# Kernel tuning notes

Hardware: AMD Instinct MI355X
Metric: run time of the kernel (lower is better)

The kernel has to match this reference:

```python
import jax, jax.numpy as jnp
import numpy as np

NUM_HEADS = 8


def setup_inputs() -> dict:
    key = jax.random.key(0)
    N, D = 131072, 512
    ks = jax.random.split(key, 10)
    inv = 1.0 / np.sqrt(D)
    return {
        "unit_embeddings": jax.random.normal(ks[0], (N, D), dtype=jnp.float32),
        "mask": jnp.ones((N,), dtype=bool),
        "mil_query": jax.random.normal(ks[1], (D,), dtype=jnp.float32),
        "Wq": jax.random.uniform(ks[2], (D, D), jnp.float32, -inv, inv),
        "bq": jax.random.uniform(ks[3], (D,), jnp.float32, -inv, inv),
        "Wk": jax.random.uniform(ks[4], (D, D), jnp.float32, -inv, inv),
        "bk": jax.random.uniform(ks[5], (D,), jnp.float32, -inv, inv),
        "Wv": jax.random.uniform(ks[6], (D, D), jnp.float32, -inv, inv),
        "bv": jax.random.uniform(ks[7], (D,), jnp.float32, -inv, inv),
        "Wo": jax.random.uniform(ks[8], (D, D), jnp.float32, -inv, inv),
        "bo": jax.random.uniform(ks[9], (D,), jnp.float32, -inv, inv),
    }


def reference(unit_embeddings, mask, mil_query, Wq, bq, Wk, bk, Wv, bv, Wo, bo):
    N, D = unit_embeddings.shape
    H = NUM_HEADS
    hd = D // H
    scale = np.float32(np.sqrt(hd))
    # The torch module expands a single learned query to N copies and takes the
    # diagonal of the NxN per-head score matrix; mathematically scores[h,n] = q_h . k_h[n] / scale.
    q = mil_query @ Wq.T + bq                       # (D,)
    K = unit_embeddings @ Wk.T + bk                 # (N, D)
    V = unit_embeddings @ Wv.T + bv                 # (N, D)
    qh = q.reshape(H, hd)                           # (H, hd)
    Kh = K.reshape(N, H, hd)
    Vh = V.reshape(N, H, hd)
    scores = jnp.einsum('hd,nhd->hn', qh, Kh) / scale   # (H, N)
    scores = jnp.where(mask[None, :], scores, -jnp.inf)
    w = jax.nn.softmax(scores, axis=-1)             # (H, N); dropout is identity at eval
    weighted = jnp.einsum('hn,nhd->hd', w, Vh)      # (H, hd)
    # torch does .transpose(0,1).contiguous().view(D): flatten in (hd, H) order
    flat = weighted.T.reshape(D)
    package_embedding = flat @ Wo.T + bo            # (D,)
    final_attention_weights = w.mean(axis=0)        # (N,)
    return package_embedding, final_attention_weights
```

## Files before the change

### kernel.cpp

```cpp
#include <hip/hip_runtime.h>

#define NN 131072
#define DD 512
#define HH 8
#define NUNIT 2048

__device__ __forceinline__ float wave_sum64(float x) {
  float t;
#define DPPADD(ctrl)                                                                     \
  t = __int_as_float(__builtin_amdgcn_update_dpp(0, __float_as_int(x), ctrl, 0xf, 0xf, true)); \
  x += t;
  DPPADD(0x111)
  DPPADD(0x112)
  DPPADD(0x114)
  DPPADD(0x118)
  DPPADD(0x142)
  DPPADD(0x143)
#undef DPPADD
  return x;
}

__device__ __forceinline__ float rdlane(float v, int l) {
  return __int_as_float(__builtin_amdgcn_readlane(__float_as_int(v), l));
}

__device__ __forceinline__ float dpp_xor1(float x) {
  return __int_as_float(__builtin_amdgcn_update_dpp(0, __float_as_int(x), 0xB1, 0xf, 0xf, true));
}
__device__ __forceinline__ float dpp_xor2(float x) {
  return __int_as_float(__builtin_amdgcn_update_dpp(0, __float_as_int(x), 0x4E, 0xf, 0xf, true));
}

__global__ __launch_bounds__(256) void kA_q(const float* __restrict__ Wq,
                                            const float* __restrict__ bq,
                                            const float* __restrict__ mq,
                                            float* __restrict__ q) {
  int lane = threadIdx.x & 63;
  int gw = blockIdx.x * 4 + (threadIdx.x >> 6);
  const float4* wr = (const float4*)(Wq + (size_t)gw * DD);
  const float4* m4 = (const float4*)mq;
  float4 w0 = wr[lane], w1 = wr[64 + lane];
  float4 m0 = m4[lane], m1 = m4[64 + lane];
  float p = w0.x * m0.x + w0.y * m0.y + w0.z * m0.z + w0.w * m0.w +
            w1.x * m1.x + w1.y * m1.y + w1.z * m1.z + w1.w * m1.w;
  p = wave_sum64(p);
  if (lane == 63) q[gw] = p + bq[gw];
}

__global__ __launch_bounds__(256) void kB_kq(const float* __restrict__ Wk,
                                             const float* __restrict__ bk,
                                             const float* __restrict__ q,
                                             float* __restrict__ kq,
                                             float* __restrict__ cq) {
  int T = blockIdx.x * 256 + threadIdx.x;
  int h = T >> 9, j = T & 511;
  float acc = 0.f;
#pragma unroll 8
  for (int d = 0; d < 64; ++d)
    acc += q[h * 64 + d] * Wk[(size_t)(h * 64 + d) * DD + j];
  kq[T] = acc;
  if (T < HH) {
    float c = 0.f;
    for (int d = 0; d < 64; ++d) c += q[T * 64 + d] * bk[T * 64 + d];
    cq[T] = c;
  }
}

__global__ __launch_bounds__(256, 4) void kFused(const float* __restrict__ emb,
                                                 const float* __restrict__ kqg,
                                                 const float* __restrict__ cqp,
                                                 float* __restrict__ scoresT,
                                                 float2* __restrict__ mz_part,
                                                 float* __restrict__ part) {
  const int lane = threadIdx.x & 63;
  const int wid = threadIdx.x >> 6;
  const int pair = wid >> 1;
  const int half = wid & 1;
  const int u = blockIdx.x * 2 + pair;
  const int hbase = half * 4;

  float c[4][8];
#pragma unroll
  for (int hh = 0; hh < 4; ++hh) {
    int h = hbase + hh;
    float4 x = *(const float4*)(kqg + h * 512 + 4 * lane);
    float4 y = *(const float4*)(kqg + h * 512 + 256 + 4 * lane);
    c[hh][0] = x.x; c[hh][1] = x.y; c[hh][2] = x.z; c[hh][3] = x.w;
    c[hh][4] = y.x; c[hh][5] = y.y; c[hh][6] = y.z; c[hh][7] = y.w;
  }
  const float cq_v = cqp[hbase + (lane & 3)];

  float acc[4][8];
#pragma unroll
  for (int hh = 0; hh < 4; ++hh)
#pragma unroll
    for (int k = 0; k < 8; ++k) acc[hh][k] = 0.f;
  float m_v = -3.0e38f;
  float z_v = 0.f;

  const float4* e4 = (const float4*)emb + (size_t)u * 64 * 128;

#pragma unroll 1
  for (int tile = 0; tile < 32; ++tile) {
    float4 ea0 = e4[(tile * 2 + 0) * 128 + lane];
    float4 eb0 = e4[(tile * 2 + 0) * 128 + 64 + lane];
    float4 ea1 = e4[(tile * 2 + 1) * 128 + lane];
    float4 eb1 = e4[(tile * 2 + 1) * 128 + 64 + lane];

    float s[8];
#pragma unroll
    for (int hh = 0; hh < 4; ++hh) {
      s[hh] = ea0.x * c[hh][0] + ea0.y * c[hh][1] + ea0.z * c[hh][2] + ea0.w * c[hh][3] +
              eb0.x * c[hh][4] + eb0.y * c[hh][5] + eb0.z * c[hh][6] + eb0.w * c[hh][7];
      s[4 + hh] = ea1.x * c[hh][0] + ea1.y * c[hh][1] + ea1.z * c[hh][2] + ea1.w * c[hh][3] +
                  eb1.x * c[hh][4] + eb1.y * c[hh][5] + eb1.z * c[hh][6] + eb1.w * c[hh][7];
    }

    float v;
    {
      float r4[4];
#pragma unroll
      for (int j = 0; j < 4; ++j) {
        float mine = (lane & 1) ? s[2 * j + 1] : s[2 * j];
        float send = (lane & 1) ? s[2 * j] : s[2 * j + 1];
        r4[j] = mine + dpp_xor1(send);
      }
      float r2[2];
#pragma unroll
      for (int j = 0; j < 2; ++j) {
        float mine = (lane & 2) ? r4[2 * j + 1] : r4[2 * j];
        float send = (lane & 2) ? r4[2 * j] : r4[2 * j + 1];
        r2[j] = mine + dpp_xor2(send);
      }
      float mine = (lane & 4) ? r2[1] : r2[0];
      float send = (lane & 4) ? r2[0] : r2[1];
      v = mine + __shfl_xor(send, 4, 64);
      v += __shfl_xor(v, 8, 64);
      v += __shfl_xor(v, 16, 64);
      v += __shfl_xor(v, 32, 64);
    }
    v = (v + cq_v) * 0.125f;

    if (lane < 8)
      scoresT[(size_t)(u * 64 + tile * 2 + (lane >> 2)) * 8 + hbase + (lane & 3)] = v;

    float tmax = fmaxf(v, __shfl_xor(v, 4, 64));
    if (__any(tmax > m_v + 8.0f)) {
      float m_new = fmaxf(m_v, tmax);
      float f = __expf(m_v - m_new);
      z_v *= f;
      m_v = m_new;
#pragma unroll
      for (int hh = 0; hh < 4; ++hh) {
        float fh = rdlane(f, hh);
        acc[hh][0] *= fh; acc[hh][1] *= fh; acc[hh][2] *= fh; acc[hh][3] *= fh;
        acc[hh][4] *= fh; acc[hh][5] *= fh; acc[hh][6] *= fh; acc[hh][7] *= fh;
      }
    }
    float w = __expf(v - m_v);
    z_v += w;

#pragma unroll
    for (int hh = 0; hh < 4; ++hh) {
      float w0 = rdlane(w, hh);
      acc[hh][0] += w0 * ea0.x; acc[hh][1] += w0 * ea0.y;
      acc[hh][2] += w0 * ea0.z; acc[hh][3] += w0 * ea0.w;
      acc[hh][4] += w0 * eb0.x; acc[hh][5] += w0 * eb0.y;
      acc[hh][6] += w0 * eb0.z; acc[hh][7] += w0 * eb0.w;
      float w1 = rdlane(w, 4 + hh);
      acc[hh][0] += w1 * ea1.x; acc[hh][1] += w1 * ea1.y;
      acc[hh][2] += w1 * ea1.z; acc[hh][3] += w1 * ea1.w;
      acc[hh][4] += w1 * eb1.x; acc[hh][5] += w1 * eb1.y;
      acc[hh][6] += w1 * eb1.z; acc[hh][7] += w1 * eb1.w;
    }
  }

  float zc = z_v + __shfl_xor(z_v, 4, 64);
  if (lane < 4) mz_part[(size_t)u * 8 + hbase + lane] = make_float2(m_v, zc);

#pragma unroll
  for (int hh = 0; hh < 4; ++hh) {
    float4 v0 = make_float4(acc[hh][0], acc[hh][1], acc[hh][2], acc[hh][3]);
    float4 v1 = make_float4(acc[hh][4], acc[hh][5], acc[hh][6], acc[hh][7]);
    *(float4*)(part + (size_t)u * 4096 + (hbase + hh) * 512 + 4 * lane) = v0;
    *(float4*)(part + (size_t)u * 4096 + (hbase + hh) * 512 + 256 + 4 * lane) = v1;
  }
}

__device__ __forceinline__ float2 mz_combine(float2 A, float2 B) {
  float M = fmaxf(A.x, B.x);
  float Z = A.y * __expf(A.x - M) + B.y * __expf(B.x - M);
  return make_float2(M, Z);
}

__global__ __launch_bounds__(256) void kMZ(const float2* __restrict__ mzp,
                                           float2* __restrict__ mzf) {
  __shared__ float2 red[256];
  int t = threadIdx.x, h = blockIdx.x;
  float2 acc = make_float2(-3.0e38f, 0.f);
  for (int i = t; i < NUNIT; i += 256) acc = mz_combine(acc, mzp[(size_t)i * 8 + h]);
  red[t] = acc;
  __syncthreads();
  for (int off = 128; off >= 1; off >>= 1) {
    if (t < off) red[t] = mz_combine(red[t], red[t + off]);
    __syncthreads();
  }
  if (t == 0) mzf[h] = make_float2(red[0].x, 1.0f / red[0].y);
}

__global__ __launch_bounds__(256) void kC1(const float* __restrict__ part,
                                           const float2* __restrict__ mzp,
                                           const float2* __restrict__ mzf,
                                           float* __restrict__ part2) {
  __shared__ float f_lds[64];
  int t = threadIdx.x;
  int bc = blockIdx.x & 31, oc = blockIdx.x >> 5;
  int h = oc >> 1;
  float2 MZ = mzf[h];
  if (t < 64) {
    float2 mz = mzp[(size_t)(bc * 64 + t) * 8 + h];
    f_lds[t] = __expf(mz.x - MZ.x) * MZ.y;
  }
  __syncthreads();
  int idx = oc * 256 + t;
  float acc = 0.f;
#pragma unroll 4
  for (int j = 0; j < 64; ++j)
    acc += f_lds[j] * part[(size_t)(bc * 64 + j) * 4096 + idx];
  part2[(size_t)bc * 4096 + idx] = acc;
}

__global__ __launch_bounds__(256) void kC2(const float* __restrict__ part2,
                                           float* __restrict__ s_final) {
  int idx = blockIdx.x * 256 + threadIdx.x;
  float acc = 0.f;
#pragma unroll 8
  for (int bc = 0; bc < 32; ++bc) acc += part2[(size_t)bc * 4096 + idx];
  s_final[idx] = acc;
}

__global__ __launch_bounds__(256) void kFAW(const float* __restrict__ scoresT,
                                            const float2* __restrict__ mzf,
                                            float* __restrict__ faw) {
  int n = blockIdx.x * 256 + threadIdx.x;
  float4 s0 = *(const float4*)(scoresT + (size_t)n * 8);
  float4 s1 = *(const float4*)(scoresT + (size_t)n * 8 + 4);
  float sv[8] = {s0.x, s0.y, s0.z, s0.w, s1.x, s1.y, s1.z, s1.w};
  float sum = 0.f;
#pragma unroll
  for (int h = 0; h < 8; ++h) {
    float2 mz = mzf[h];
    sum += __expf(sv[h] - mz.x) * mz.y;
  }
  faw[n] = sum * 0.125f;
}

__global__ __launch_bounds__(256) void kP5a(const float* __restrict__ Wv,
                                            const float* __restrict__ bv,
                                            const float* __restrict__ s_final,
                                            float* __restrict__ flat) {
  int lane = threadIdx.x & 63;
  int r = blockIdx.x * 4 + (threadIdx.x >> 6);
  int h = r >> 6, i = r & 63;
  const float4* wr = (const float4*)(Wv + (size_t)r * 512);
  const float4* sh = (const float4*)(s_final + h * 512);
  float4 w0 = wr[lane], w1 = wr[64 + lane];
  float4 s0 = sh[lane], s1 = sh[64 + lane];
  float p = w0.x * s0.x + w0.y * s0.y + w0.z * s0.z + w0.w * s0.w +
            w1.x * s1.x + w1.y * s1.y + w1.z * s1.z + w1.w * s1.w;
  p = wave_sum64(p);
  if (lane == 63) flat[i * 8 + h] = p + bv[r];
}

__global__ __launch_bounds__(256) void kP5b(const float* __restrict__ Wo,
                                            const float* __restrict__ bo,
                                            const float* __restrict__ flat,
                                            float* __restrict__ out) {
  int lane = threadIdx.x & 63;
  int d = blockIdx.x * 4 + (threadIdx.x >> 6);
  const float4* wr = (const float4*)(Wo + (size_t)d * 512);
  const float4* fl = (const float4*)flat;
  float4 w0 = wr[lane], w1 = wr[64 + lane];
  float4 f0 = fl[lane], f1 = fl[64 + lane];
  float p = w0.x * f0.x + w0.y * f0.y + w0.z * f0.z + w0.w * f0.w +
            w1.x * f1.x + w1.y * f1.y + w1.z * f1.z + w1.w * f1.w;
  p = wave_sum64(p);
  if (lane == 63) out[d] = p + bo[d];
}

extern "C" void kernel_launch(void* const* d_in, const int* in_sizes, int n_in,
                              void* d_out, int out_size, void* d_ws, size_t ws_size,
                              hipStream_t stream) {
  const float* emb = (const float*)d_in[0];
  const float* mq = (const float*)d_in[2];
  const float* Wq = (const float*)d_in[3];
  const float* bq = (const float*)d_in[4];
  const float* Wk = (const float*)d_in[5];
  const float* bk = (const float*)d_in[6];
  const float* Wv = (const float*)d_in[7];
  const float* bv = (const float*)d_in[8];
  const float* Wo = (const float*)d_in[9];
  const float* bo = (const float*)d_in[10];
  float* out = (float*)d_out;
  float* ws = (float*)d_ws;

  float* q = ws + 0;
  float* kq = ws + 512;
  float* cq = ws + 4608;
  float2* mz_part = (float2*)(ws + 4624);
  float2* mz_final = (float2*)(ws + 37392);
  float* s_final = ws + 37408;
  float* flat = ws + 41504;
  float* scoresT = ws + 42016;
  float* part2 = ws + 1090592;
  float* part = ws + 1221664;

  hipLaunchKernelGGL(kA_q, dim3(128), dim3(256), 0, stream, Wq, bq, mq, q);
  hipLaunchKernelGGL(kB_kq, dim3(16), dim3(256), 0, stream, Wk, bk, q, kq, cq);
  hipLaunchKernelGGL(kFused, dim3(1024), dim3(256), 0, stream, emb, kq, cq, scoresT,
                     mz_part, part);
  hipLaunchKernelGGL(kMZ, dim3(8), dim3(256), 0, stream, mz_part, mz_final);
  hipLaunchKernelGGL(kC1, dim3(512), dim3(256), 0, stream, part, mz_part, mz_final, part2);
  hipLaunchKernelGGL(kC2, dim3(16), dim3(256), 0, stream, part2, s_final);
  hipLaunchKernelGGL(kFAW, dim3(512), dim3(256), 0, stream, scoresT, mz_final, out + 512);
  hipLaunchKernelGGL(kP5a, dim3(128), dim3(256), 0, stream, Wv, bv, s_final, flat);
  hipLaunchKernelGGL(kP5b, dim3(128), dim3(256), 0, stream, Wo, bo, flat, out);
}
```

Baseline: 97.71 us.

## Split heads across four waves per unit and double-buffer embedding tile loads

Each block now covers one 64-row unit, and each of its four waves handles two heads instead of four, so the grid doubles to 2048 blocks. Per-wave register use for weights and accumulators is halved, and the reduction tree gets shorter. The tile loop is unrolled by two with ping-pong register buffers so the next tile's loads are in flight while the current tile is processed. In exchange, each embedding row is now read by four waves instead of two, raising L2/global traffic, and the extra buffers add register pressure.

```diff
diff --git a/kernel.cpp b/kernel.cpp
--- a/kernel.cpp
+++ b/kernel.cpp
@@ -74,25 +74,23 @@
                                                  float* __restrict__ part) {
   const int lane = threadIdx.x & 63;
   const int wid = threadIdx.x >> 6;
-  const int pair = wid >> 1;
-  const int half = wid & 1;
-  const int u = blockIdx.x * 2 + pair;
-  const int hbase = half * 4;
-
-  float c[4][8];
-#pragma unroll
-  for (int hh = 0; hh < 4; ++hh) {
+  const int u = blockIdx.x;
+  const int hbase = wid * 2;
+
+  float c[2][8];
+#pragma unroll
+  for (int hh = 0; hh < 2; ++hh) {
     int h = hbase + hh;
     float4 x = *(const float4*)(kqg + h * 512 + 4 * lane);
     float4 y = *(const float4*)(kqg + h * 512 + 256 + 4 * lane);
     c[hh][0] = x.x; c[hh][1] = x.y; c[hh][2] = x.z; c[hh][3] = x.w;
     c[hh][4] = y.x; c[hh][5] = y.y; c[hh][6] = y.z; c[hh][7] = y.w;
   }
-  const float cq_v = cqp[hbase + (lane & 3)];
-
-  float acc[4][8];
-#pragma unroll
-  for (int hh = 0; hh < 4; ++hh)
+  const float cq_v = cqp[hbase + (lane & 1)];
+
+  float acc[2][8];
+#pragma unroll
+  for (int hh = 0; hh < 2; ++hh)
 #pragma unroll
     for (int k = 0; k < 8; ++k) acc[hh][k] = 0.f;
   float m_v = -3.0e38f;
@@ -100,86 +98,86 @@
 
   const float4* e4 = (const float4*)emb + (size_t)u * 64 * 128;
 
+  float4 Aa0, Ab0, Aa1, Ab1;
+  float4 Ba0, Bb0, Ba1, Bb1;
+
+#define LOADT(Pa0, Pb0, Pa1, Pb1, t)                 \
+  do {                                               \
+    Pa0 = e4[((t) * 2 + 0) * 128 + lane];            \
+    Pb0 = e4[((t) * 2 + 0) * 128 + 64 + lane];       \
+    Pa1 = e4[((t) * 2 + 1) * 128 + lane];            \
+    Pb1 = e4[((t) * 2 + 1) * 128 + 64 + lane];       \
+  } while (0)
+
+#define PROCT(Pa0, Pb0, Pa1, Pb1, t)                                                        \
+  do {                                                                                      \
+    float s0, s1, s2, s3;                                                                   \
+    s0 = Pa0.x * c[0][0] + Pa0.y * c[0][1] + Pa0.z * c[0][2] + Pa0.w * c[0][3] +            \
+         Pb0.x * c[0][4] + Pb0.y * c[0][5] + Pb0.z * c[0][6] + Pb0.w * c[0][7];             \
+    s1 = Pa0.x * c[1][0] + Pa0.y * c[1][1] + Pa0.z * c[1][2] + Pa0.w * c[1][3] +            \
+         Pb0.x * c[1][4] + Pb0.y * c[1][5] + Pb0.z * c[1][6] + Pb0.w * c[1][7];             \
+    s2 = Pa1.x * c[0][0] + Pa1.y * c[0][1] + Pa1.z * c[0][2] + Pa1.w * c[0][3] +            \
+         Pb1.x * c[0][4] + Pb1.y * c[0][5] + Pb1.z * c[0][6] + Pb1.w * c[0][7];             \
+    s3 = Pa1.x * c[1][0] + Pa1.y * c[1][1] + Pa1.z * c[1][2] + Pa1.w * c[1][3] +            \
+         Pb1.x * c[1][4] + Pb1.y * c[1][5] + Pb1.z * c[1][6] + Pb1.w * c[1][7];             \
+                                                                 \
+    float m0 = (lane & 1) ? s1 : s0, d0 = (lane & 1) ? s0 : s1;                             \
+    float m1 = (lane & 1) ? s3 : s2, d1 = (lane & 1) ? s2 : s3;                             \
+    float r0 = m0 + dpp_xor1(d0);                                                           \
+    float r1 = m1 + dpp_xor1(d1);                                                           \
+                                                                  \
+    float mm = (lane & 2) ? r1 : r0, dd = (lane & 2) ? r0 : r1;                             \
+    float v = mm + dpp_xor2(dd);                                                            \
+                                                                         \
+    v += __shfl_xor(v, 4, 64);                                                              \
+    v += __shfl_xor(v, 8, 64);                                                              \
+    v += __shfl_xor(v, 16, 64);                                                             \
+    v += __shfl_xor(v, 32, 64);                                                             \
+    v = (v + cq_v) * 0.125f;   \
+    if (lane < 4)                                                                           \
+      scoresT[(size_t)(u * 64 + (t) * 2 + (lane >> 1)) * 8 + hbase + (lane & 1)] = v;       \
+    float tmax = fmaxf(v, __shfl_xor(v, 2, 64));                     \
+    if (__any(tmax > m_v + 8.0f)) {                           \
+      float m_new = fmaxf(m_v, tmax);                                                       \
+      float f = __expf(m_v - m_new);                                                        \
+      z_v *= f;                                                                             \
+      m_v = m_new;                                                                          \
+      float f0 = rdlane(f, 0), f1 = rdlane(f, 1);                                           \
+      acc[0][0] *= f0; acc[0][1] *= f0; acc[0][2] *= f0; acc[0][3] *= f0;                   \
+      acc[0][4] *= f0; acc[0][5] *= f0; acc[0][6] *= f0; acc[0][7] *= f0;                   \
+      acc[1][0] *= f1; acc[1][1] *= f1; acc[1][2] *= f1; acc[1][3] *= f1;                   \
+      acc[1][4] *= f1; acc[1][5] *= f1; acc[1][6] *= f1; acc[1][7] *= f1;                   \
+    }                                                                                       \
+    float w = __expf(v - m_v);                                                              \
+    z_v += w;                                                                               \
+    float w00 = rdlane(w, 0), w01 = rdlane(w, 1);                                           \
+    float w10 = rdlane(w, 2), w11 = rdlane(w, 3);                                           \
+    acc[0][0] += w00 * Pa0.x + w10 * Pa1.x; acc[0][1] += w00 * Pa0.y + w10 * Pa1.y;         \
+    acc[0][2] += w00 * Pa0.z + w10 * Pa1.z; acc[0][3] += w00 * Pa0.w + w10 * Pa1.w;         \
+    acc[0][4] += w00 * Pb0.x + w10 * Pb1.x; acc[0][5] += w00 * Pb0.y + w10 * Pb1.y;         \
+    acc[0][6] += w00 * Pb0.z + w10 * Pb1.z; acc[0][7] += w00 * Pb0.w + w10 * Pb1.w;         \
+    acc[1][0] += w01 * Pa0.x + w11 * Pa1.x; acc[1][1] += w01 * Pa0.y + w11 * Pa1.y;         \
+    acc[1][2] += w01 * Pa0.z + w11 * Pa1.z; acc[1][3] += w01 * Pa0.w + w11 * Pa1.w;         \
+    acc[1][4] += w01 * Pb0.x + w11 * Pb1.x; acc[1][5] += w01 * Pb0.y + w11 * Pb1.y;         \
+    acc[1][6] += w01 * Pb0.z + w11 * Pb1.z; acc[1][7] += w01 * Pb0.w + w11 * Pb1.w;         \
+  } while (0)
+
+  LOADT(Aa0, Ab0, Aa1, Ab1, 0);
 #pragma unroll 1
-  for (int tile = 0; tile < 32; ++tile) {
-    float4 ea0 = e4[(tile * 2 + 0) * 128 + lane];
-    float4 eb0 = e4[(tile * 2 + 0) * 128 + 64 + lane];
-    float4 ea1 = e4[(tile * 2 + 1) * 128 + lane];
-    float4 eb1 = e4[(tile * 2 + 1) * 128 + 64 + lane];
-
-    float s[8];
-#pragma unroll
-    for (int hh = 0; hh < 4; ++hh) {
-      s[hh] = ea0.x * c[hh][0] + ea0.y * c[hh][1] + ea0.z * c[hh][2] + ea0.w * c[hh][3] +
-              eb0.x * c[hh][4] + eb0.y * c[hh][5] + eb0.z * c[hh][6] + eb0.w * c[hh][7];
-      s[4 + hh] = ea1.x * c[hh][0] + ea1.y * c[hh][1] + ea1.z * c[hh][2] + ea1.w * c[hh][3] +
-                  eb1.x * c[hh][4] + eb1.y * c[hh][5] + eb1.z * c[hh][6] + eb1.w * c[hh][7];
-    }
-
-    float v;
-    {
-      float r4[4];
-#pragma unroll
-      for (int j = 0; j < 4; ++j) {
-        float mine = (lane & 1) ? s[2 * j + 1] : s[2 * j];
-        float send = (lane & 1) ? s[2 * j] : s[2 * j + 1];
-        r4[j] = mine + dpp_xor1(send);
-      }
-      float r2[2];
-#pragma unroll
-      for (int j = 0; j < 2; ++j) {
-        float mine = (lane & 2) ? r4[2 * j + 1] : r4[2 * j];
-        float send = (lane & 2) ? r4[2 * j] : r4[2 * j + 1];
-        r2[j] = mine + dpp_xor2(send);
-      }
-      float mine = (lane & 4) ? r2[1] : r2[0];
-      float send = (lane & 4) ? r2[0] : r2[1];
-      v = mine + __shfl_xor(send, 4, 64);
-      v += __shfl_xor(v, 8, 64);
-      v += __shfl_xor(v, 16, 64);
-      v += __shfl_xor(v, 32, 64);
-    }
-    v = (v + cq_v) * 0.125f;
-
-    if (lane < 8)
-      scoresT[(size_t)(u * 64 + tile * 2 + (lane >> 2)) * 8 + hbase + (lane & 3)] = v;
-
-    float tmax = fmaxf(v, __shfl_xor(v, 4, 64));
-    if (__any(tmax > m_v + 8.0f)) {
-      float m_new = fmaxf(m_v, tmax);
-      float f = __expf(m_v - m_new);
-      z_v *= f;
-      m_v = m_new;
-#pragma unroll
-      for (int hh = 0; hh < 4; ++hh) {
-        float fh = rdlane(f, hh);
-        acc[hh][0] *= fh; acc[hh][1] *= fh; acc[hh][2] *= fh; acc[hh][3] *= fh;
-        acc[hh][4] *= fh; acc[hh][5] *= fh; acc[hh][6] *= fh; acc[hh][7] *= fh;
-      }
-    }
-    float w = __expf(v - m_v);
-    z_v += w;
-
-#pragma unroll
-    for (int hh = 0; hh < 4; ++hh) {
-      float w0 = rdlane(w, hh);
-      acc[hh][0] += w0 * ea0.x; acc[hh][1] += w0 * ea0.y;
-      acc[hh][2] += w0 * ea0.z; acc[hh][3] += w0 * ea0.w;
-      acc[hh][4] += w0 * eb0.x; acc[hh][5] += w0 * eb0.y;
-      acc[hh][6] += w0 * eb0.z; acc[hh][7] += w0 * eb0.w;
-      float w1 = rdlane(w, 4 + hh);
-      acc[hh][0] += w1 * ea1.x; acc[hh][1] += w1 * ea1.y;
-      acc[hh][2] += w1 * ea1.z; acc[hh][3] += w1 * ea1.w;
-      acc[hh][4] += w1 * eb1.x; acc[hh][5] += w1 * eb1.y;
-      acc[hh][6] += w1 * eb1.z; acc[hh][7] += w1 * eb1.w;
-    }
-  }
-
-  float zc = z_v + __shfl_xor(z_v, 4, 64);
-  if (lane < 4) mz_part[(size_t)u * 8 + hbase + lane] = make_float2(m_v, zc);
-
-#pragma unroll
-  for (int hh = 0; hh < 4; ++hh) {
+  for (int tp = 0; tp < 16; ++tp) {
+    LOADT(Ba0, Bb0, Ba1, Bb1, 2 * tp + 1);
+    PROCT(Aa0, Ab0, Aa1, Ab1, 2 * tp);
+    if (tp < 15) LOADT(Aa0, Ab0, Aa1, Ab1, 2 * tp + 2);
+    PROCT(Ba0, Bb0, Ba1, Bb1, 2 * tp + 1);
+  }
+#undef LOADT
+#undef PROCT
+
+  float zc = z_v + __shfl_xor(z_v, 2, 64);
+  if (lane < 2) mz_part[(size_t)u * 8 + hbase + lane] = make_float2(m_v, zc);
+
+#pragma unroll
+  for (int hh = 0; hh < 2; ++hh) {
     float4 v0 = make_float4(acc[hh][0], acc[hh][1], acc[hh][2], acc[hh][3]);
     float4 v1 = make_float4(acc[hh][4], acc[hh][5], acc[hh][6], acc[hh][7]);
     *(float4*)(part + (size_t)u * 4096 + (hbase + hh) * 512 + 4 * lane) = v0;
@@ -317,7 +315,7 @@
 
   hipLaunchKernelGGL(kA_q, dim3(128), dim3(256), 0, stream, Wq, bq, mq, q);
   hipLaunchKernelGGL(kB_kq, dim3(16), dim3(256), 0, stream, Wk, bk, q, kq, cq);
-  hipLaunchKernelGGL(kFused, dim3(1024), dim3(256), 0, stream, emb, kq, cq, scoresT,
+  hipLaunchKernelGGL(kFused, dim3(2048), dim3(256), 0, stream, emb, kq, cq, scoresT,
                      mz_part, part);
   hipLaunchKernelGGL(kMZ, dim3(8), dim3(256), 0, stream, mz_part, mz_final);
   hipLaunchKernelGGL(kC1, dim3(512), dim3(256), 0, stream, part, mz_part, mz_final, part2);
```

After: 112.7 us. 1.15x slower.

## Stage embedding rows through LDS with async global_load_lds pipeline

Applied to the files above, without the earlier changes.

The fused score/softmax/accumulate kernel now streams 8-row chunks of embeddings into a 4-slot LDS ring buffer using async global-to-LDS loads, three chunks ahead. All four waves in a block share each chunk, with each wave handling two heads instead of four. Each block now covers 256 rows, so there are 512 partials and the combine kernels shrink to match. The aim is to hide global memory latency and read each embedding row from HBM only once per block, instead of having head-split waves fetch the same rows separately. The cost is a barrier per chunk, hand-tuned vmcnt waits that must match the load counts exactly, and 64KB of LDS per block, which lowers occupancy.

```diff
diff --git a/kernel.cpp b/kernel.cpp
--- a/kernel.cpp
+++ b/kernel.cpp
@@ -3,7 +3,7 @@
 #define NN 131072
 #define DD 512
 #define HH 8
-#define NUNIT 2048
+#define NPART 512
 
 __device__ __forceinline__ float wave_sum64(float x) {
   float t;
@@ -66,120 +66,137 @@
   }
 }
 
-__global__ __launch_bounds__(256, 4) void kFused(const float* __restrict__ emb,
+__global__ __launch_bounds__(256, 2) void kFused(const float* __restrict__ emb,
                                                  const float* __restrict__ kqg,
                                                  const float* __restrict__ cqp,
                                                  float* __restrict__ scoresT,
                                                  float2* __restrict__ mz_part,
                                                  float* __restrict__ part) {
+  __shared__ float lds[4 * 4096];
+
   const int lane = threadIdx.x & 63;
   const int wid = threadIdx.x >> 6;
-  const int pair = wid >> 1;
-  const int half = wid & 1;
-  const int u = blockIdx.x * 2 + pair;
-  const int hbase = half * 4;
-
-  float c[4][8];
-#pragma unroll
-  for (int hh = 0; hh < 4; ++hh) {
+  const int u = blockIdx.x;
+  const int hbase = wid * 2;
+  const size_t rowbase = (size_t)u * 256;
+
+  float c[2][8];
+#pragma unroll
+  for (int hh = 0; hh < 2; ++hh) {
     int h = hbase + hh;
     float4 x = *(const float4*)(kqg + h * 512 + 4 * lane);
     float4 y = *(const float4*)(kqg + h * 512 + 256 + 4 * lane);
     c[hh][0] = x.x; c[hh][1] = x.y; c[hh][2] = x.z; c[hh][3] = x.w;
     c[hh][4] = y.x; c[hh][5] = y.y; c[hh][6] = y.z; c[hh][7] = y.w;
   }
-  const float cq_v = cqp[hbase + (lane & 3)];
-
-  float acc[4][8];
-#pragma unroll
-  for (int hh = 0; hh < 4; ++hh)
+  const float cq_v = cqp[hbase + (lane & 1)];
+  asm volatile("s_waitcnt vmcnt(0)" ::: "memory");
+
+  float acc[2][8];
+#pragma unroll
+  for (int hh = 0; hh < 2; ++hh)
 #pragma unroll
     for (int k = 0; k < 8; ++k) acc[hh][k] = 0.f;
   float m_v = -3.0e38f;
   float z_v = 0.f;
 
-  const float4* e4 = (const float4*)emb + (size_t)u * 64 * 128;
+#define STAGE(ch)                                                                        \
+  do {                                                                                   \
+    int slot_ = (ch) & 3;                                                                \
+    const float* gsrc_ = emb + (rowbase + (size_t)(ch) * 8) * 512 + wid * 1024;          \
+    float* ldst_ = &lds[slot_ * 4096 + wid * 1024];                                      \
+    _Pragma("unroll")                                                                    \
+    for (int i_ = 0; i_ < 4; ++i_) {                                                     \
+      __builtin_amdgcn_global_load_lds(                                                  \
+          (const __attribute__((address_space(1))) void*)(gsrc_ + i_ * 256 + lane * 4),  \
+          (__attribute__((address_space(3))) void*)(ldst_ + i_ * 256), 16, 0, 0);        \
+    }                                                                                    \
+  } while (0)
+
+  STAGE(0);
+  STAGE(1);
+  STAGE(2);
 
 #pragma unroll 1
-  for (int tile = 0; tile < 32; ++tile) {
-    float4 ea0 = e4[(tile * 2 + 0) * 128 + lane];
-    float4 eb0 = e4[(tile * 2 + 0) * 128 + 64 + lane];
-    float4 ea1 = e4[(tile * 2 + 1) * 128 + lane];
-    float4 eb1 = e4[(tile * 2 + 1) * 128 + 64 + lane];
-
-    float s[8];
-#pragma unroll
-    for (int hh = 0; hh < 4; ++hh) {
-      s[hh] = ea0.x * c[hh][0] + ea0.y * c[hh][1] + ea0.z * c[hh][2] + ea0.w * c[hh][3] +
-              eb0.x * c[hh][4] + eb0.y * c[hh][5] + eb0.z * c[hh][6] + eb0.w * c[hh][7];
-      s[4 + hh] = ea1.x * c[hh][0] + ea1.y * c[hh][1] + ea1.z * c[hh][2] + ea1.w * c[hh][3] +
-                  eb1.x * c[hh][4] + eb1.y * c[hh][5] + eb1.z * c[hh][6] + eb1.w * c[hh][7];
+  for (int ch = 0; ch < 32; ++ch) {
+    if (ch == 0 || ch == 31) {
+      asm volatile("s_waitcnt vmcnt(8)" ::: "memory");
+    } else if (ch == 1 || ch == 30) {
+      asm volatile("s_waitcnt vmcnt(12)" ::: "memory");
+    } else {
+      asm volatile("s_waitcnt vmcnt(16)" ::: "memory");
     }
-
-    float v;
-    {
-      float r4[4];
-#pragma unroll
-      for (int j = 0; j < 4; ++j) {
-        float mine = (lane & 1) ? s[2 * j + 1] : s[2 * j];
-        float send = (lane & 1) ? s[2 * j] : s[2 * j + 1];
-        r4[j] = mine + dpp_xor1(send);
-      }
-      float r2[2];
-#pragma unroll
-      for (int j = 0; j < 2; ++j) {
-        float mine = (lane & 2) ? r4[2 * j + 1] : r4[2 * j];
-        float send = (lane & 2) ? r4[2 * j] : r4[2 * j + 1];
-        r2[j] = mine + dpp_xor2(send);
-      }
-      float mine = (lane & 4) ? r2[1] : r2[0];
-      float send = (lane & 4) ? r2[0] : r2[1];
-      v = mine + __shfl_xor(send, 4, 64);
+    __builtin_amdgcn_s_barrier();
+    asm volatile("" ::: "memory");
+
+    if (ch + 3 < 32) STAGE(ch + 3);
+
+    const float* sl = &lds[(ch & 3) * 4096];
+#pragma unroll
+    for (int st = 0; st < 4; ++st) {
+      float4 ea0 = *(const float4*)(sl + (st * 2 + 0) * 512 + 4 * lane);
+      float4 eb0 = *(const float4*)(sl + (st * 2 + 0) * 512 + 256 + 4 * lane);
+      float4 ea1 = *(const float4*)(sl + (st * 2 + 1) * 512 + 4 * lane);
+      float4 eb1 = *(const float4*)(sl + (st * 2 + 1) * 512 + 256 + 4 * lane);
+
+      float s0 = ea0.x * c[0][0] + ea0.y * c[0][1] + ea0.z * c[0][2] + ea0.w * c[0][3] +
+                 eb0.x * c[0][4] + eb0.y * c[0][5] + eb0.z * c[0][6] + eb0.w * c[0][7];
+      float s1 = ea0.x * c[1][0] + ea0.y * c[1][1] + ea0.z * c[1][2] + ea0.w * c[1][3] +
+                 eb0.x * c[1][4] + eb0.y * c[1][5] + eb0.z * c[1][6] + eb0.w * c[1][7];
+      float s2 = ea1.x * c[0][0] + ea1.y * c[0][1] + ea1.z * c[0][2] + ea1.w * c[0][3] +
+                 eb1.x * c[0][4] + eb1.y * c[0][5] + eb1.z * c[0][6] + eb1.w * c[0][7];
+      float s3 = ea1.x * c[1][0] + ea1.y * c[1][1] + ea1.z * c[1][2] + ea1.w * c[1][3] +
+                 eb1.x * c[1][4] + eb1.y * c[1][5] + eb1.z * c[1][6] + eb1.w * c[1][7];
+
+      float m0 = (lane & 1) ? s1 : s0, d0 = (lane & 1) ? s0 : s1;
+      float m1 = (lane & 1) ? s3 : s2, d1 = (lane & 1) ? s2 : s3;
+      float r0 = m0 + dpp_xor1(d0);
+      float r1 = m1 + dpp_xor1(d1);
+      float mm = (lane & 2) ? r1 : r0, dd = (lane & 2) ? r0 : r1;
+      float v = mm + dpp_xor2(dd);
+      v += __shfl_xor(v, 4, 64);
       v += __shfl_xor(v, 8, 64);
       v += __shfl_xor(v, 16, 64);
       v += __shfl_xor(v, 32, 64);
+      v = (v + cq_v) * 0.125f;
+
+      int row = ch * 8 + st * 2;
+      if (lane < 4)
+        scoresT[(rowbase + row + (lane >> 1)) * 8 + hbase + (lane & 1)] = v;
+
+      float tmax = fmaxf(v, __shfl_xor(v, 2, 64));
+      if (__any(tmax > m_v + 8.0f)) {
+        float m_new = fmaxf(m_v, tmax);
+        float f = __expf(m_v - m_new);
+        z_v *= f;
+        m_v = m_new;
+        float f0 = rdlane(f, 0), f1 = rdlane(f, 1);
+        acc[0][0] *= f0; acc[0][1] *= f0; acc[0][2] *= f0; acc[0][3] *= f0;
+        acc[0][4] *= f0; acc[0][5] *= f0; acc[0][6] *= f0; acc[0][7] *= f0;
+        acc[1][0] *= f1; acc[1][1] *= f1; acc[1][2] *= f1; acc[1][3] *= f1;
+        acc[1][4] *= f1; acc[1][5] *= f1; acc[1][6] *= f1; acc[1][7] *= f1;
+      }
+      float w = __expf(v - m_v);
+      z_v += w;
+      float w00 = rdlane(w, 0), w01 = rdlane(w, 1);
+      float w10 = rdlane(w, 2), w11 = rdlane(w, 3);
+      acc[0][0] += w00 * ea0.x + w10 * ea1.x; acc[0][1] += w00 * ea0.y + w10 * ea1.y;
+      acc[0][2] += w00 * ea0.z + w10 * ea1.z; acc[0][3] += w00 * ea0.w + w10 * ea1.w;
+      acc[0][4] += w00 * eb0.x + w10 * eb1.x; acc[0][5] += w00 * eb0.y + w10 * eb1.y;
+      acc[0][6] += w00 * eb0.z + w10 * eb1.z; acc[0][7] += w00 * eb0.w + w10 * eb1.w;
+      acc[1][0] += w01 * ea0.x + w11 * ea1.x; acc[1][1] += w01 * ea0.y + w11 * ea1.y;
+      acc[1][2] += w01 * ea0.z + w11 * ea1.z; acc[1][3] += w01 * ea0.w + w11 * ea1.w;
+      acc[1][4] += w01 * eb0.x + w11 * eb1.x; acc[1][5] += w01 * eb0.y + w11 * eb1.y;
+      acc[1][6] += w01 * eb0.z + w11 * eb1.z; acc[1][7] += w01 * eb0.w + w11 * eb1.w;
     }
-    v = (v + cq_v) * 0.125f;
-
-    if (lane < 8)
-      scoresT[(size_t)(u * 64 + tile * 2 + (lane >> 2)) * 8 + hbase + (lane & 3)] = v;
-
-    float tmax = fmaxf(v, __shfl_xor(v, 4, 64));
-    if (__any(tmax > m_v + 8.0f)) {
-      float m_new = fmaxf(m_v, tmax);
-      float f = __expf(m_v - m_new);
-      z_v *= f;
-      m_v = m_new;
-#pragma unroll
-      for (int hh = 0; hh < 4; ++hh) {
-        float fh = rdlane(f, hh);
-        acc[hh][0] *= fh; acc[hh][1] *= fh; acc[hh][2] *= fh; acc[hh][3] *= fh;
-        acc[hh][4] *= fh; acc[hh][5] *= fh; acc[hh][6] *= fh; acc[hh][7] *= fh;
-      }
-    }
-    float w = __expf(v - m_v);
-    z_v += w;
-
-#pragma unroll
-    for (int hh = 0; hh < 4; ++hh) {
-      float w0 = rdlane(w, hh);
-      acc[hh][0] += w0 * ea0.x; acc[hh][1] += w0 * ea0.y;
-      acc[hh][2] += w0 * ea0.z; acc[hh][3] += w0 * ea0.w;
-      acc[hh][4] += w0 * eb0.x; acc[hh][5] += w0 * eb0.y;
-      acc[hh][6] += w0 * eb0.z; acc[hh][7] += w0 * eb0.w;
-      float w1 = rdlane(w, 4 + hh);
-      acc[hh][0] += w1 * ea1.x; acc[hh][1] += w1 * ea1.y;
-      acc[hh][2] += w1 * ea1.z; acc[hh][3] += w1 * ea1.w;
-      acc[hh][4] += w1 * eb1.x; acc[hh][5] += w1 * eb1.y;
-      acc[hh][6] += w1 * eb1.z; acc[hh][7] += w1 * eb1.w;
-    }
-  }
-
-  float zc = z_v + __shfl_xor(z_v, 4, 64);
-  if (lane < 4) mz_part[(size_t)u * 8 + hbase + lane] = make_float2(m_v, zc);
-
-#pragma unroll
-  for (int hh = 0; hh < 4; ++hh) {
+  }
+#undef STAGE
+
+  float zc = z_v + __shfl_xor(z_v, 2, 64);
+  if (lane < 2) mz_part[(size_t)u * 8 + hbase + lane] = make_float2(m_v, zc);
+
+#pragma unroll
+  for (int hh = 0; hh < 2; ++hh) {
     float4 v0 = make_float4(acc[hh][0], acc[hh][1], acc[hh][2], acc[hh][3]);
     float4 v1 = make_float4(acc[hh][4], acc[hh][5], acc[hh][6], acc[hh][7]);
     *(float4*)(part + (size_t)u * 4096 + (hbase + hh) * 512 + 4 * lane) = v0;
@@ -198,7 +215,7 @@
   __shared__ float2 red[256];
   int t = threadIdx.x, h = blockIdx.x;
   float2 acc = make_float2(-3.0e38f, 0.f);
-  for (int i = t; i < NUNIT; i += 256) acc = mz_combine(acc, mzp[(size_t)i * 8 + h]);
+  for (int i = t; i < NPART; i += 256) acc = mz_combine(acc, mzp[(size_t)i * 8 + h]);
   red[t] = acc;
   __syncthreads();
   for (int off = 128; off >= 1; off >>= 1) {
@@ -212,21 +229,21 @@
                                            const float2* __restrict__ mzp,
                                            const float2* __restrict__ mzf,
                                            float* __restrict__ part2) {
-  __shared__ float f_lds[64];
+  __shared__ float f_lds[16];
   int t = threadIdx.x;
   int bc = blockIdx.x & 31, oc = blockIdx.x >> 5;
   int h = oc >> 1;
   float2 MZ = mzf[h];
-  if (t < 64) {
-    float2 mz = mzp[(size_t)(bc * 64 + t) * 8 + h];
+  if (t < 16) {
+    float2 mz = mzp[(size_t)(bc * 16 + t) * 8 + h];
     f_lds[t] = __expf(mz.x - MZ.x) * MZ.y;
   }
   __syncthreads();
   int idx = oc * 256 + t;
   float acc = 0.f;
 #pragma unroll 4
-  for (int j = 0; j < 64; ++j)
-    acc += f_lds[j] * part[(size_t)(bc * 64 + j) * 4096 + idx];
+  for (int j = 0; j < 16; ++j)
+    acc += f_lds[j] * part[(size_t)(bc * 16 + j) * 4096 + idx];
   part2[(size_t)bc * 4096 + idx] = acc;
 }
 
@@ -308,16 +325,16 @@
   float* kq = ws + 512;
   float* cq = ws + 4608;
   float2* mz_part = (float2*)(ws + 4624);
-  float2* mz_final = (float2*)(ws + 37392);
-  float* s_final = ws + 37408;
-  float* flat = ws + 41504;
-  float* scoresT = ws + 42016;
-  float* part2 = ws + 1090592;
-  float* part = ws + 1221664;
+  float2* mz_final = (float2*)(ws + 12816);
+  float* s_final = ws + 12832;
+  float* flat = ws + 16928;
+  float* scoresT = ws + 17440;
+  float* part2 = ws + 1066016;
+  float* part = ws + 1197088;
 
   hipLaunchKernelGGL(kA_q, dim3(128), dim3(256), 0, stream, Wq, bq, mq, q);
   hipLaunchKernelGGL(kB_kq, dim3(16), dim3(256), 0, stream, Wk, bk, q, kq, cq);
-  hipLaunchKernelGGL(kFused, dim3(1024), dim3(256), 0, stream, emb, kq, cq, scoresT,
+  hipLaunchKernelGGL(kFused, dim3(512), dim3(256), 0, stream, emb, kq, cq, scoresT,
                      mz_part, part);
   hipLaunchKernelGGL(kMZ, dim3(8), dim3(256), 0, stream, mz_part, mz_final);
   hipLaunchKernelGGL(kC1, dim3(512), dim3(256), 0, stream, part, mz_part, mz_final, part2);
```

Result: slower. 119.5 us (+22.3%).
